# Performance work log

Hardware: AMD Instinct MI355X
Metric: run time of the kernel (lower is better)

## Reference

```python
import jax, jax.numpy as jnp
import numpy as np

N_HEADS = 16

def setup_inputs() -> dict:
    key = jax.random.key(0)
    ks = jax.random.split(key, 7)
    B, S, D = 2, 2048, 1024
    sc = 0.02
    return {
        "x": jax.random.normal(ks[0], (B, S, D), dtype=jnp.float32),
        "Wq": jax.random.normal(ks[1], (D, D), dtype=jnp.float32) * sc,
        "bq": jax.random.normal(ks[2], (D,), dtype=jnp.float32) * sc,
        "Wk": jax.random.normal(ks[3], (D, D), dtype=jnp.float32) * sc,
        "bk": jax.random.normal(ks[4], (D,), dtype=jnp.float32) * sc,
        "Wv": jax.random.normal(ks[5], (D, D), dtype=jnp.float32) * sc,
        "bv": jax.random.normal(ks[6], (D,), dtype=jnp.float32) * sc,
    }

def reference(x, Wq, bq, Wk, bk, Wv, bv):
    B, S, D = x.shape
    H = N_HEADS
    W = D // H  # head width
    # torch Linear: y = x @ W.T + b
    q = x @ Wq.T + bq
    k = x @ Wk.T + bk
    v = x @ Wv.T + bv
    # split last dim into (H, W) and move heads forward: (B, H, S, W)
    q = q.reshape(B, S, H, W).transpose(0, 2, 1, 3)
    k = k.reshape(B, S, H, W).transpose(0, 2, 1, 3)
    v = v.reshape(B, S, H, W).transpose(0, 2, 1, 3)
    scores = jnp.einsum("bhqw,bhkw->bhqk", q, k) / jnp.sqrt(jnp.asarray(W, x.dtype))
    # original applies softmax, (dropout=identity at eval), then softmax AGAIN
    scores = jax.nn.softmax(scores, axis=-1)
    scores = jax.nn.softmax(scores, axis=-1)
    h = jnp.einsum("bhqk,bhkw->bhqw", scores, v)
    h = h.transpose(0, 2, 1, 3).reshape(B, S, D)
    return h
```

## Files before the change

kernel.cpp:

```cpp
#include <hip/hip_runtime.h>
#include <cstdint>
#include <cstddef>

typedef __bf16 bf16_t;
typedef __bf16 bf16x4 __attribute__((ext_vector_type(4)));
typedef __bf16 bf16x8 __attribute__((ext_vector_type(8)));
typedef float f32x4 __attribute__((ext_vector_type(4)));

typedef __attribute__((address_space(1))) unsigned int gu32;
typedef __attribute__((address_space(3))) unsigned int lu32;

#define MFMA16(a, b, c) __builtin_amdgcn_mfma_f32_16x16x32_bf16((a), (b), (c), 0, 0, 0)

__device__ __forceinline__ void gload_lds16(const void* g, void* l) {
    __builtin_amdgcn_global_load_lds((gu32*)const_cast<void*>(g), (lu32*)l, 16, 0, 0);
}

__global__ __launch_bounds__(256) void cvt_bf16(
    const float* __restrict__ x, const float* __restrict__ Wq,
    const float* __restrict__ Wk, const float* __restrict__ Wv,
    bf16_t* __restrict__ xb, bf16_t* __restrict__ Wqb,
    bf16_t* __restrict__ Wkb, bf16_t* __restrict__ Wvb)
{
    const int z = blockIdx.z;
    const float* src = (z == 0) ? x : (z == 1) ? Wq : (z == 2) ? Wk : Wv;
    bf16_t* dst      = (z == 0) ? xb : (z == 1) ? Wqb : (z == 2) ? Wkb : Wvb;
    const int n = (z == 0) ? 4096 * 1024 : 1024 * 1024;
    const int stride = gridDim.x * blockDim.x * 4;
    for (int i = (blockIdx.x * blockDim.x + threadIdx.x) * 4; i < n; i += stride) {
        const float4 f = *(const float4*)(src + i);
        bf16x4 o; o[0] = (bf16_t)f.x; o[1] = (bf16_t)f.y; o[2] = (bf16_t)f.z; o[3] = (bf16_t)f.w;
        *(bf16x4*)(dst + i) = o;
    }
}

__global__ __launch_bounds__(512) void qkv_gemm_bf16(
    const bf16_t* __restrict__ xb,
    const bf16_t* __restrict__ W0b, const float* __restrict__ b0,
    const bf16_t* __restrict__ W1b, const float* __restrict__ b1,
    const bf16_t* __restrict__ W2b, const float* __restrict__ b2,
    bf16_t* __restrict__ Qo, bf16_t* __restrict__ Ko, bf16_t* __restrict__ VTo)
{
    const int z = blockIdx.z;
    const bf16_t* Wm = (z == 0) ? W0b : (z == 1) ? W1b : W2b;
    const float* bia = (z == 0) ? b0 : (z == 1) ? b1 : b2;

    __shared__ bf16_t As[2][128 * 32];
    __shared__ bf16_t Bs[2][128 * 32];

    const int tid  = threadIdx.x;
    const int lane = tid & 63;
    const int wv   = tid >> 6;
    const int quad = lane >> 4;
    const int l16  = lane & 15;
    const int wm   = wv >> 1;
    const int wn   = wv & 1;
    const int m0   = blockIdx.x * 128;
    const int n0   = blockIdx.y * 128;

    const int rs = tid >> 2;
    const int gs = ((tid & 3) ^ ((rs >> 1) & 3)) * 8;
    const int fp = (quad ^ ((l16 >> 1) & 3)) * 8;

    f32x4 acc[2][4];
    for (int i = 0; i < 2; i++)
        for (int j = 0; j < 4; j++) acc[i][j] = (f32x4)0.0f;

    gload_lds16(xb + (size_t)(m0 + rs) * 1024 + gs, &As[0][(wv * 64) * 8]);
    gload_lds16(Wm + (size_t)(n0 + rs) * 1024 + gs, &Bs[0][(wv * 64) * 8]);

#pragma unroll 2
    for (int kt = 0; kt < 32; kt++) {
        const int cur = kt & 1, nxt = cur ^ 1;
        __syncthreads();
        if (kt < 31) {
            const int kp = (kt + 1) * 32;
            gload_lds16(xb + (size_t)(m0 + rs) * 1024 + kp + gs, &As[nxt][(wv * 64) * 8]);
            gload_lds16(Wm + (size_t)(n0 + rs) * 1024 + kp + gs, &Bs[nxt][(wv * 64) * 8]);
        }
        bf16x8 af[2], bfr[4];
        for (int mt = 0; mt < 2; mt++)
            af[mt] = *(const bf16x8*)&As[cur][(wm * 32 + mt * 16 + l16) * 32 + fp];
        for (int nt = 0; nt < 4; nt++)
            bfr[nt] = *(const bf16x8*)&Bs[cur][(wn * 64 + nt * 16 + l16) * 32 + fp];
        for (int mt = 0; mt < 2; mt++)
            for (int nt = 0; nt < 4; nt++)
                acc[mt][nt] = MFMA16(af[mt], bfr[nt], acc[mt][nt]);
    }

    float bv[4];
    for (int nt = 0; nt < 4; nt++)
        bv[nt] = bia[n0 + wn * 64 + nt * 16 + l16];

    if (z < 2) {
        bf16_t* out = (z == 0) ? Qo : Ko;
        for (int mt = 0; mt < 2; mt++) {
            const int mrow = m0 + wm * 32 + mt * 16 + quad * 4;
            for (int nt = 0; nt < 4; nt++) {
                const int n = n0 + wn * 64 + nt * 16 + l16;
                for (int r = 0; r < 4; r++)
                    out[(size_t)(mrow + r) * 1024 + n] = (bf16_t)(acc[mt][nt][r] + bv[nt]);
            }
        }
    } else {
        const int h = blockIdx.y * 2 + wn;
        for (int mt = 0; mt < 2; mt++) {
            const int sg = m0 + wm * 32 + mt * 16 + quad * 4;
            const int b  = sg >> 11;
            const int s  = sg & 2047;
            for (int nt = 0; nt < 4; nt++) {
                const int w = nt * 16 + l16;
                bf16x4 pk;
                for (int r = 0; r < 4; r++) pk[r] = (bf16_t)(acc[mt][nt][r] + bv[nt]);
                *(bf16x4*)(VTo + ((size_t)((b * 16 + h) * 64 + w)) * 2048 + s) = pk;
            }
        }
    }
}

__global__ __launch_bounds__(512) void attn(
    const bf16_t* __restrict__ Qg, const bf16_t* __restrict__ Kg,
    const bf16_t* __restrict__ VTg, float* __restrict__ out)
{
    const int qt = blockIdx.x;
    const int h  = blockIdx.y;
    const int b  = blockIdx.z;

    const int tid  = threadIdx.x;
    const int wv   = tid >> 6;
    const int lane = tid & 63;
    const int quad = lane >> 4;
    const int l16  = lane & 15;

    const size_t base  = ((size_t)b * 2048) * 1024 + (size_t)h * 64;
    const size_t vbase = ((size_t)(b * 16 + h) * 64) * 2048;
    const int q0 = qt * 128;

    __shared__ bf16_t PQ[128 * 64];
    __shared__ bf16_t Ks[2][64 * 64];
    __shared__ bf16_t Vs[2][64 * 64];

    {
        const int c0 = tid, c1 = 512 + tid;
        const int r0 = c0 >> 3, g0 = ((c0 & 7) ^ (r0 & 7)) * 8;
        const int r1 = c1 >> 3, g1 = ((c1 & 7) ^ (r1 & 7)) * 8;
        gload_lds16(Qg + base + (size_t)(q0 + r0) * 1024 + g0, PQ + (wv * 64) * 8);
        gload_lds16(Qg + base + (size_t)(q0 + r1) * 1024 + g1, PQ + (512 + wv * 64) * 8);
    }
    const int rk = tid >> 3;
    const int gk = ((tid & 7) ^ (rk & 7)) * 8;
    gload_lds16(Kg + base + (size_t)rk * 1024 + gk, &Ks[0][(wv * 64) * 8]);
    gload_lds16(VTg + vbase + (size_t)rk * 2048 + gk, &Vs[0][(wv * 64) * 8]);

    const int fs0 = ((0 ^ quad) ^ (l16 & 7)) * 8;
    const int fs1 = ((4 ^ quad) ^ (l16 & 7)) * 8;
    const int rowA = (wv * 16 + l16) * 64;

    const int qrow = wv * 16 + l16;

    f32x4 oa[4], vsacc[4], l1acc;
    for (int nt = 0; nt < 4; nt++) { oa[nt] = (f32x4)0.0f; vsacc[nt] = (f32x4)0.0f; }
    l1acc = (f32x4)0.0f;

    bf16x8 ones;
    for (int j = 0; j < 8; j++) ones[j] = (bf16_t)1.0f;

    __syncthreads();
    const bf16x8 aq0 = *(const bf16x8*)&PQ[rowA + fs0];
    const bf16x8 aq1 = *(const bf16x8*)&PQ[rowA + fs1];

#pragma unroll 2
    for (int kt = 0; kt < 32; kt++) {
        const int cur = kt & 1, nxt = cur ^ 1;
        __syncthreads();

        if (kt < 31) {
            gload_lds16(Kg + base + (size_t)((kt + 1) * 64 + rk) * 1024 + gk,
                        &Ks[nxt][(wv * 64) * 8]);
            gload_lds16(VTg + vbase + (size_t)rk * 2048 + (kt + 1) * 64 + gk,
                        &Vs[nxt][(wv * 64) * 8]);
        }

        f32x4 sa[4];
        for (int nt = 0; nt < 4; nt++) sa[nt] = (f32x4)0.0f;
        for (int nt = 0; nt < 4; nt++) {
            bf16x8 kb = *(const bf16x8*)&Ks[cur][(nt * 16 + l16) * 64 + fs0];
            sa[nt] = MFMA16(kb, aq0, sa[nt]);
        }
        for (int nt = 0; nt < 4; nt++) {
            bf16x8 kb = *(const bf16x8*)&Ks[cur][(nt * 16 + l16) * 64 + fs1];
            sa[nt] = MFMA16(kb, aq1, sa[nt]);
        }

        for (int nt = 0; nt < 4; nt++) {
            bf16x4 pk;
            for (int r = 0; r < 4; r++)
                pk[r] = (bf16_t)__expf(sa[nt][r] * 0.125f);
            const int c = nt * 2 + (quad >> 1);
            *(bf16x4*)&PQ[qrow * 64 + ((c ^ (qrow & 7)) * 8) + (quad & 1) * 4] = pk;
        }

        bf16x8 bv0[4], bv1[4];
        for (int nt = 0; nt < 4; nt++)
            bv0[nt] = *(const bf16x8*)&Vs[cur][(nt * 16 + l16) * 64 + fs0];
        for (int nt = 0; nt < 4; nt++)
            bv1[nt] = *(const bf16x8*)&Vs[cur][(nt * 16 + l16) * 64 + fs1];
        for (int nt = 0; nt < 4; nt++) vsacc[nt] = MFMA16(ones, bv0[nt], vsacc[nt]);
        for (int nt = 0; nt < 4; nt++) vsacc[nt] = MFMA16(ones, bv1[nt], vsacc[nt]);

        {
            bf16x8 af = *(const bf16x8*)&PQ[rowA + fs0];
            l1acc = MFMA16(af, ones, l1acc);
            for (int nt = 0; nt < 4; nt++)
                oa[nt] = MFMA16(af, bv0[nt], oa[nt]);
        }
        {
            bf16x8 af = *(const bf16x8*)&PQ[rowA + fs1];
            l1acc = MFMA16(af, ones, l1acc);
            for (int nt = 0; nt < 4; nt++)
                oa[nt] = MFMA16(af, bv1[nt], oa[nt]);
        }
    }

    float invq[4];
    for (int r = 0; r < 4; r++) invq[r] = 1.0f / l1acc[r];

    const float inv_denom = 1.0f / 2049.0f;
    for (int nt = 0; nt < 4; nt++) {
        for (int r = 0; r < 4; r++) {
            const int srow = q0 + wv * 16 + quad * 4 + r;
            out[((size_t)b * 2048 + srow) * 1024 + (size_t)h * 64 + nt * 16 + l16] =
                (vsacc[nt][0] + oa[nt][r] * invq[r]) * inv_denom;
        }
    }
}

extern "C" void kernel_launch(void* const* d_in, const int* in_sizes, int n_in,
                              void* d_out, int out_size, void* d_ws, size_t ws_size,
                              hipStream_t stream) {
    const float* x  = (const float*)d_in[0];
    const float* Wq = (const float*)d_in[1];
    const float* bq = (const float*)d_in[2];
    const float* Wk = (const float*)d_in[3];
    const float* bk = (const float*)d_in[4];
    const float* Wv = (const float*)d_in[5];
    const float* bv = (const float*)d_in[6];

    bf16_t* Qw  = (bf16_t*)d_ws;
    bf16_t* Kw  = Qw + (size_t)4096 * 1024;
    bf16_t* VTw = Kw + (size_t)4096 * 1024;

    bf16_t* xb  = (bf16_t*)d_out;
    bf16_t* Wqb = xb + (size_t)4096 * 1024;
    bf16_t* Wkb = Wqb + (size_t)1024 * 1024;
    bf16_t* Wvb = Wkb + (size_t)1024 * 1024;

    cvt_bf16<<<dim3(1024, 1, 4), 256, 0, stream>>>(x, Wq, Wk, Wv, xb, Wqb, Wkb, Wvb);
    qkv_gemm_bf16<<<dim3(32, 8, 3), 512, 0, stream>>>(
        xb, Wqb, bq, Wkb, bk, Wvb, bv, Qw, Kw, VTw);
    attn<<<dim3(16, 16, 2), 512, 0, stream>>>(Qw, Kw, VTw, (float*)d_out);
}
```

Baseline: 172.7 us.

## Precompute V column sums in GEMM epilogue and software-pipeline attention P·V

The V projection epilogue now reduces per-block partial column sums of V into a small workspace, which the attention kernel sums at the end. This replaces the per-iteration ones·V MFMA accumulation with a single final lookup. The attention loop is also restructured with a double-buffered P tile, so the P·V MFMAs of the previous tile overlap the QK MFMAs and exp of the current one. It also sets a min-blocks occupancy hint on launch_bounds. The costs are extra LDS, register pressure from holding V fragments across iterations, and an extra reduction and sync in the GEMM.

Result: faster. 166.7 us (-3.5%).

```diff
diff --git a/kernel.cpp b/kernel.cpp
--- a/kernel.cpp
+++ b/kernel.cpp
@@ -39,7 +39,8 @@
     const bf16_t* __restrict__ W0b, const float* __restrict__ b0,
     const bf16_t* __restrict__ W1b, const float* __restrict__ b1,
     const bf16_t* __restrict__ W2b, const float* __restrict__ b2,
-    bf16_t* __restrict__ Qo, bf16_t* __restrict__ Ko, bf16_t* __restrict__ VTo)
+    bf16_t* __restrict__ Qo, bf16_t* __restrict__ Ko, bf16_t* __restrict__ VTo,
+    float* __restrict__ Vp)
 {
     const int z = blockIdx.z;
     const bf16_t* Wm = (z == 0) ? W0b : (z == 1) ? W1b : W2b;
@@ -104,23 +105,48 @@
         }
     } else {
         const int h = blockIdx.y * 2 + wn;
+        float psum[4] = {0.f, 0.f, 0.f, 0.f};
         for (int mt = 0; mt < 2; mt++) {
             const int sg = m0 + wm * 32 + mt * 16 + quad * 4;
-            const int b  = sg >> 11;
+            const int bb = sg >> 11;
             const int s  = sg & 2047;
             for (int nt = 0; nt < 4; nt++) {
                 const int w = nt * 16 + l16;
                 bf16x4 pk;
-                for (int r = 0; r < 4; r++) pk[r] = (bf16_t)(acc[mt][nt][r] + bv[nt]);
-                *(bf16x4*)(VTo + ((size_t)((b * 16 + h) * 64 + w)) * 2048 + s) = pk;
+                for (int r = 0; r < 4; r++) {
+                    pk[r] = (bf16_t)(acc[mt][nt][r] + bv[nt]);
+                    psum[nt] += (float)pk[r];
+                }
+                *(bf16x4*)(VTo + ((size_t)((bb * 16 + h) * 64 + w)) * 2048 + s) = pk;
             }
         }
-    }
-}
-
-__global__ __launch_bounds__(512) void attn(
+        for (int nt = 0; nt < 4; nt++) {
+            psum[nt] += __shfl_xor(psum[nt], 16, 64);
+            psum[nt] += __shfl_xor(psum[nt], 32, 64);
+        }
+        float* red = (float*)&As[0][0];
+        if (quad == 0)
+            for (int nt = 0; nt < 4; nt++)
+                red[(wv * 4 + nt) * 16 + l16] = psum[nt];
+        __syncthreads();
+        if (wm == 0 && quad == 0) {
+            const int bb = m0 >> 11;
+            const int j  = blockIdx.x & 15;
+            for (int nt = 0; nt < 4; nt++) {
+                float s4 = ((red[((wn + 0) * 4 + nt) * 16 + l16]
+                           + red[((wn + 2) * 4 + nt) * 16 + l16])
+                           + red[((wn + 4) * 4 + nt) * 16 + l16])
+                           + red[((wn + 6) * 4 + nt) * 16 + l16];
+                Vp[((size_t)((bb * 16 + h) * 64 + nt * 16 + l16)) * 16 + j] = s4;
+            }
+        }
+    }
+}
+
+__global__ __launch_bounds__(512, 4) void attn(
     const bf16_t* __restrict__ Qg, const bf16_t* __restrict__ Kg,
-    const bf16_t* __restrict__ VTg, float* __restrict__ out)
+    const bf16_t* __restrict__ VTg, const float* __restrict__ Vp,
+    float* __restrict__ out)
 {
     const int qt = blockIdx.x;
     const int h  = blockIdx.y;
@@ -136,7 +162,7 @@
     const size_t vbase = ((size_t)(b * 16 + h) * 64) * 2048;
     const int q0 = qt * 128;
 
-    __shared__ bf16_t PQ[128 * 64];
+    __shared__ bf16_t Ps[2][128 * 64];
     __shared__ bf16_t Ks[2][64 * 64];
     __shared__ bf16_t Vs[2][64 * 64];
 
@@ -144,8 +170,8 @@
         const int c0 = tid, c1 = 512 + tid;
         const int r0 = c0 >> 3, g0 = ((c0 & 7) ^ (r0 & 7)) * 8;
         const int r1 = c1 >> 3, g1 = ((c1 & 7) ^ (r1 & 7)) * 8;
-        gload_lds16(Qg + base + (size_t)(q0 + r0) * 1024 + g0, PQ + (wv * 64) * 8);
-        gload_lds16(Qg + base + (size_t)(q0 + r1) * 1024 + g1, PQ + (512 + wv * 64) * 8);
+        gload_lds16(Qg + base + (size_t)(q0 + r0) * 1024 + g0, &Ps[0][(wv * 64) * 8]);
+        gload_lds16(Qg + base + (size_t)(q0 + r1) * 1024 + g1, &Ps[0][(512 + wv * 64) * 8]);
     }
     const int rk = tid >> 3;
     const int gk = ((tid & 7) ^ (rk & 7)) * 8;
@@ -155,82 +181,123 @@
     const int fs0 = ((0 ^ quad) ^ (l16 & 7)) * 8;
     const int fs1 = ((4 ^ quad) ^ (l16 & 7)) * 8;
     const int rowA = (wv * 16 + l16) * 64;
-
     const int qrow = wv * 16 + l16;
 
-    f32x4 oa[4], vsacc[4], l1acc;
-    for (int nt = 0; nt < 4; nt++) { oa[nt] = (f32x4)0.0f; vsacc[nt] = (f32x4)0.0f; }
+    f32x4 oa[4], l1acc;
+    for (int nt = 0; nt < 4; nt++) oa[nt] = (f32x4)0.0f;
     l1acc = (f32x4)0.0f;
 
     bf16x8 ones;
     for (int j = 0; j < 8; j++) ones[j] = (bf16_t)1.0f;
 
     __syncthreads();
-    const bf16x8 aq0 = *(const bf16x8*)&PQ[rowA + fs0];
-    const bf16x8 aq1 = *(const bf16x8*)&PQ[rowA + fs1];
-
-#pragma unroll 2
-    for (int kt = 0; kt < 32; kt++) {
-        const int cur = kt & 1, nxt = cur ^ 1;
-        __syncthreads();
-
-        if (kt < 31) {
-            gload_lds16(Kg + base + (size_t)((kt + 1) * 64 + rk) * 1024 + gk,
-                        &Ks[nxt][(wv * 64) * 8]);
-            gload_lds16(VTg + vbase + (size_t)rk * 2048 + (kt + 1) * 64 + gk,
-                        &Vs[nxt][(wv * 64) * 8]);
-        }
+    const bf16x8 aq0 = *(const bf16x8*)&Ps[0][rowA + fs0];
+    const bf16x8 aq1 = *(const bf16x8*)&Ps[0][rowA + fs1];
+
+    bf16x8 bv0[4], bv1[4];
+
+    {
+        gload_lds16(Kg + base + (size_t)(64 + rk) * 1024 + gk, &Ks[1][(wv * 64) * 8]);
+        gload_lds16(VTg + vbase + (size_t)rk * 2048 + 64 + gk, &Vs[1][(wv * 64) * 8]);
 
         f32x4 sa[4];
         for (int nt = 0; nt < 4; nt++) sa[nt] = (f32x4)0.0f;
         for (int nt = 0; nt < 4; nt++) {
-            bf16x8 kb = *(const bf16x8*)&Ks[cur][(nt * 16 + l16) * 64 + fs0];
+            bf16x8 kb = *(const bf16x8*)&Ks[0][(nt * 16 + l16) * 64 + fs0];
             sa[nt] = MFMA16(kb, aq0, sa[nt]);
         }
         for (int nt = 0; nt < 4; nt++) {
-            bf16x8 kb = *(const bf16x8*)&Ks[cur][(nt * 16 + l16) * 64 + fs1];
+            bf16x8 kb = *(const bf16x8*)&Ks[0][(nt * 16 + l16) * 64 + fs1];
             sa[nt] = MFMA16(kb, aq1, sa[nt]);
         }
-
         for (int nt = 0; nt < 4; nt++) {
             bf16x4 pk;
             for (int r = 0; r < 4; r++)
                 pk[r] = (bf16_t)__expf(sa[nt][r] * 0.125f);
             const int c = nt * 2 + (quad >> 1);
-            *(bf16x4*)&PQ[qrow * 64 + ((c ^ (qrow & 7)) * 8) + (quad & 1) * 4] = pk;
-        }
-
-        bf16x8 bv0[4], bv1[4];
+            *(bf16x4*)&Ps[0][qrow * 64 + ((c ^ (qrow & 7)) * 8) + (quad & 1) * 4] = pk;
+        }
+        for (int nt = 0; nt < 4; nt++)
+            bv0[nt] = *(const bf16x8*)&Vs[0][(nt * 16 + l16) * 64 + fs0];
+        for (int nt = 0; nt < 4; nt++)
+            bv1[nt] = *(const bf16x8*)&Vs[0][(nt * 16 + l16) * 64 + fs1];
+    }
+
+#pragma unroll 2
+    for (int kt = 1; kt < 32; kt++) {
+        const int cur = kt & 1, prv = cur ^ 1;
+        __syncthreads();
+
+        const bf16x8 af0 = *(const bf16x8*)&Ps[prv][rowA + fs0];
+        const bf16x8 af1 = *(const bf16x8*)&Ps[prv][rowA + fs1];
+
+        if (kt < 31) {
+            gload_lds16(Kg + base + (size_t)((kt + 1) * 64 + rk) * 1024 + gk,
+                        &Ks[prv][(wv * 64) * 8]);
+            gload_lds16(VTg + vbase + (size_t)rk * 2048 + (kt + 1) * 64 + gk,
+                        &Vs[prv][(wv * 64) * 8]);
+        }
+
+        f32x4 sa[4];
+        for (int nt = 0; nt < 4; nt++) sa[nt] = (f32x4)0.0f;
+        for (int nt = 0; nt < 4; nt++) {
+            bf16x8 kb = *(const bf16x8*)&Ks[cur][(nt * 16 + l16) * 64 + fs0];
+            sa[nt] = MFMA16(kb, aq0, sa[nt]);
+        }
+        for (int nt = 0; nt < 4; nt++) {
+            bf16x8 kb = *(const bf16x8*)&Ks[cur][(nt * 16 + l16) * 64 + fs1];
+            sa[nt] = MFMA16(kb, aq1, sa[nt]);
+        }
+
+        l1acc = MFMA16(af0, ones, l1acc);
+        for (int nt = 0; nt < 4; nt++) oa[nt] = MFMA16(af0, bv0[nt], oa[nt]);
+        l1acc = MFMA16(af1, ones, l1acc);
+        for (int nt = 0; nt < 4; nt++) oa[nt] = MFMA16(af1, bv1[nt], oa[nt]);
+
         for (int nt = 0; nt < 4; nt++)
             bv0[nt] = *(const bf16x8*)&Vs[cur][(nt * 16 + l16) * 64 + fs0];
         for (int nt = 0; nt < 4; nt++)
             bv1[nt] = *(const bf16x8*)&Vs[cur][(nt * 16 + l16) * 64 + fs1];
-        for (int nt = 0; nt < 4; nt++) vsacc[nt] = MFMA16(ones, bv0[nt], vsacc[nt]);
-        for (int nt = 0; nt < 4; nt++) vsacc[nt] = MFMA16(ones, bv1[nt], vsacc[nt]);
-
-        {
-            bf16x8 af = *(const bf16x8*)&PQ[rowA + fs0];
-            l1acc = MFMA16(af, ones, l1acc);
-            for (int nt = 0; nt < 4; nt++)
-                oa[nt] = MFMA16(af, bv0[nt], oa[nt]);
-        }
-        {
-            bf16x8 af = *(const bf16x8*)&PQ[rowA + fs1];
-            l1acc = MFMA16(af, ones, l1acc);
-            for (int nt = 0; nt < 4; nt++)
-                oa[nt] = MFMA16(af, bv1[nt], oa[nt]);
-        }
+
+        for (int nt = 0; nt < 4; nt++) {
+            bf16x4 pk;
+            for (int r = 0; r < 4; r++)
+                pk[r] = (bf16_t)__expf(sa[nt][r] * 0.125f);
+            const int c = nt * 2 + (quad >> 1);
+            *(bf16x4*)&Ps[cur][qrow * 64 + ((c ^ (qrow & 7)) * 8) + (quad & 1) * 4] = pk;
+        }
+    }
+
+    {
+        const bf16x8 af0 = *(const bf16x8*)&Ps[1][rowA + fs0];
+        const bf16x8 af1 = *(const bf16x8*)&Ps[1][rowA + fs1];
+        l1acc = MFMA16(af0, ones, l1acc);
+        for (int nt = 0; nt < 4; nt++) oa[nt] = MFMA16(af0, bv0[nt], oa[nt]);
+        l1acc = MFMA16(af1, ones, l1acc);
+        for (int nt = 0; nt < 4; nt++) oa[nt] = MFMA16(af1, bv1[nt], oa[nt]);
     }
 
     float invq[4];
     for (int r = 0; r < 4; r++) invq[r] = 1.0f / l1acc[r];
+
+    float vs[4];
+    {
+        const size_t vprow = (size_t)(b * 16 + h) * 64;
+        for (int nt = 0; nt < 4; nt++) {
+            const f32x4 p4 = *(const f32x4*)&Vp[(vprow + nt * 16 + l16) * 16 + quad * 4];
+            float t = (p4[0] + p4[1]) + (p4[2] + p4[3]);
+            t += __shfl_xor(t, 16, 64);
+            t += __shfl_xor(t, 32, 64);
+            vs[nt] = t;
+        }
+    }
 
     const float inv_denom = 1.0f / 2049.0f;
     for (int nt = 0; nt < 4; nt++) {
         for (int r = 0; r < 4; r++) {
             const int srow = q0 + wv * 16 + quad * 4 + r;
             out[((size_t)b * 2048 + srow) * 1024 + (size_t)h * 64 + nt * 16 + l16] =
-                (vsacc[nt][0] + oa[nt][r] * invq[r]) * inv_denom;
+                (vs[nt] + oa[nt][r] * invq[r]) * inv_denom;
         }
     }
 }
@@ -249,6 +316,7 @@
     bf16_t* Qw  = (bf16_t*)d_ws;
     bf16_t* Kw  = Qw + (size_t)4096 * 1024;
     bf16_t* VTw = Kw + (size_t)4096 * 1024;
+    float*  Vp  = (float*)(VTw + (size_t)4096 * 1024);
 
     bf16_t* xb  = (bf16_t*)d_out;
     bf16_t* Wqb = xb + (size_t)4096 * 1024;
@@ -257,6 +325,6 @@
 
     cvt_bf16<<<dim3(1024, 1, 4), 256, 0, stream>>>(x, Wq, Wk, Wv, xb, Wqb, Wkb, Wvb);
     qkv_gemm_bf16<<<dim3(32, 8, 3), 512, 0, stream>>>(
-        xb, Wqb, bq, Wkb, bk, Wvb, bv, Qw, Kw, VTw);
-    attn<<<dim3(16, 16, 2), 512, 0, stream>>>(Qw, Kw, VTw, (float*)d_out);
-}
+        xb, Wqb, bq, Wkb, bk, Wvb, bv, Qw, Kw, VTw, Vp);
+    attn<<<dim3(16, 16, 2), 512, 0, stream>>>(Qw, Kw, VTw, Vp, (float*)d_out);
+}
```
